# Kernel optimization log

Hardware: AMD Instinct MI355X
Metric: run time of the kernel (lower is better)

## Reference

```python
import jax, jax.numpy as jnp
import numpy as np

N_GRAPHS = 128


def fake_quant4(W):
    # per-tensor symmetric 4-bit weight fake-quant (brevitas-style)
    s = jnp.max(jnp.abs(W)) / 7.0
    q = jnp.clip(jnp.round(W / s), -8.0, 7.0) * s
    # STE: identity gradient through rounding
    return W + jax.lax.stop_gradient(q - W)


def gin_layer(h, src, dst, wa, ba, wb, bb, n_nodes):
    # GIN aggregation: (1+eps)*x + sum_neighbors, eps=0
    agg = jax.ops.segment_sum(h[src], dst, num_segments=n_nodes)  # [N, D]
    h = h + agg
    # int4 weight-only quantized 2-layer MLP
    h = jax.nn.relu(h @ fake_quant4(wa).T + ba)
    return h @ fake_quant4(wb).T + bb


def setup_inputs() -> dict:
    key = jax.random.key(0)
    ks = jax.random.split(key, 16)
    N, E, D = 50000, 800000, 128
    inp = {
        "x": jax.random.normal(ks[0], (N, D), jnp.float32),
        "edge_index": jax.random.randint(ks[1], (2, E), 0, N),
        "batch": jnp.sort(jax.random.randint(ks[2], (N,), 0, N_GRAPHS)),
    }
    for l in range(3):
        inp[f"w{l}a"] = jax.random.normal(ks[3 + 4 * l], (D, D), jnp.float32) * 0.05
        inp[f"b{l}a"] = jnp.zeros((D,), jnp.float32)
        inp[f"w{l}b"] = jax.random.normal(ks[4 + 4 * l], (D, D), jnp.float32) * 0.05
        inp[f"b{l}b"] = jnp.zeros((D,), jnp.float32)
    return inp


def reference(x, edge_index, batch,
              w0a, b0a, w0b, b0b,
              w1a, b1a, w1b, b1b,
              w2a, b2a, w2b, b2b):
    n_nodes = x.shape[0]
    src, dst = edge_index[0], edge_index[1]
    params = [(w0a, b0a, w0b, b0b), (w1a, b1a, w1b, b1b), (w2a, b2a, w2b, b2b)]
    h = x
    for i, (wa, ba, wb, bb) in enumerate(params):
        h = gin_layer(h, src, dst, wa, ba, wb, bb, n_nodes)
        if i < len(params) - 1:
            h = jax.nn.relu(h)  # dropout with p=0 is a no-op
    # global mean pooling over graphs (JK='last')
    sums = jax.ops.segment_sum(h, batch, num_segments=N_GRAPHS)  # [G, D]
    counts = jax.ops.segment_sum(jnp.ones((n_nodes,), h.dtype), batch, num_segments=N_GRAPHS)
    return sums / jnp.maximum(counts, 1.0)[:, None]
```

## Files before the change

kernel.cpp:

```cpp
#include <hip/hip_runtime.h>
#include <math.h>

#define D 128
#define NG 128
#define SLOTS 64

typedef __attribute__((ext_vector_type(8))) unsigned short u16x8;
typedef __attribute__((ext_vector_type(8))) short bf16x8;
typedef __attribute__((ext_vector_type(4))) float f32x4;

__device__ __forceinline__ float bf2f(unsigned short u) {
  return __uint_as_float(((unsigned int)u) << 16);
}
__device__ __forceinline__ unsigned short f2bf(float f) {
  unsigned int u = __float_as_uint(f);
  u += 0x7FFFu + ((u >> 16) & 1u);
  return (unsigned short)(u >> 16);
}

__global__ __launch_bounds__(256) void prep_kernel(
    const float* __restrict__ x, unsigned short* __restrict__ o, int n8,
    const float* __restrict__ w0, const float* __restrict__ w1,
    const float* __restrict__ w2, const float* __restrict__ w3,
    const float* __restrict__ w4, const float* __restrict__ w5,
    unsigned short* __restrict__ qout, int* __restrict__ cnt, int N) {
  int i = blockIdx.x * 256 + threadIdx.x;
  if (i < N) cnt[i] = 0;
  if (i < n8) {
    const float4* xp = reinterpret_cast<const float4*>(x) + (size_t)i * 2;
    float4 a = xp[0], b = xp[1];
    u16x8 v;
    v[0] = f2bf(a.x); v[1] = f2bf(a.y); v[2] = f2bf(a.z); v[3] = f2bf(a.w);
    v[4] = f2bf(b.x); v[5] = f2bf(b.y); v[6] = f2bf(b.z); v[7] = f2bf(b.w);
    *(reinterpret_cast<u16x8*>(o) + i) = v;
  }
  if (blockIdx.x < 6) {
    const float* w;
    switch (blockIdx.x) {
      case 0: w = w0; break;
      case 1: w = w1; break;
      case 2: w = w2; break;
      case 3: w = w3; break;
      case 4: w = w4; break;
      default: w = w5; break;
    }
    unsigned short* q = qout + (size_t)blockIdx.x * (D * D);
    __shared__ float red[256];
    float m = 0.f;
    for (int k = threadIdx.x; k < D * D; k += 256) m = fmaxf(m, fabsf(w[k]));
    red[threadIdx.x] = m;
    __syncthreads();
    for (int s = 128; s > 0; s >>= 1) {
      if (threadIdx.x < s) red[threadIdx.x] = fmaxf(red[threadIdx.x], red[threadIdx.x + s]);
      __syncthreads();
    }
    float s = red[0] / 7.0f;
    for (int k = threadIdx.x; k < D * D; k += 256) {
      float r = rintf(w[k] / s);
      r = fminf(fmaxf(r, -8.f), 7.f);
      q[k] = f2bf((s > 0.f) ? r * s : 0.f);
    }
  }
}

__global__ __launch_bounds__(256) void build_kernel(const int* __restrict__ dst,
                                                    const int* __restrict__ src,
                                                    int* __restrict__ cnt, int* __restrict__ esrc,
                                                    int E, int per_team) {
  int team = blockIdx.x & 7;
  int tb = blockIdx.x >> 3;
  int nb = gridDim.x >> 3;
  int lo = team * per_team;
  int hi = lo + per_team;
  for (int e = tb * 256 + threadIdx.x; e < E; e += nb * 256) {
    int d = dst[e];
    if (d >= lo && d < hi) {
      int slot = atomicAdd(&cnt[d], 1);
      if (slot < SLOTS) esrc[(size_t)d * SLOTS + slot] = src[e];
    }
  }
}

__global__ __launch_bounds__(256) void aggregate_kernel(
    const unsigned short* __restrict__ h, const int* __restrict__ cnt,
    const int* __restrict__ esrc, unsigned short* __restrict__ out, int n) {
  int node = blockIdx.x * 16 + threadIdx.y;
  if (node >= n) return;
  int x = threadIdx.x;
  const u16x8* hp = reinterpret_cast<const u16x8*>(h);
  u16x8 v = hp[(size_t)node * 16 + x];
  float acc[8];
#pragma unroll
  for (int i = 0; i < 8; i++) acc[i] = bf2f(v[i]);
  int c = cnt[node];
  if (c > SLOTS) c = SLOTS;
  const int* base = esrc + (size_t)node * SLOTS;
  int e = 0;
  for (; e + 8 <= c; e += 8) {
    int4 i0 = *reinterpret_cast<const int4*>(base + e);
    int4 i1 = *reinterpret_cast<const int4*>(base + e + 4);
    u16x8 a0 = hp[(size_t)i0.x * 16 + x];
    u16x8 a1 = hp[(size_t)i0.y * 16 + x];
    u16x8 a2 = hp[(size_t)i0.z * 16 + x];
    u16x8 a3 = hp[(size_t)i0.w * 16 + x];
    u16x8 a4 = hp[(size_t)i1.x * 16 + x];
    u16x8 a5 = hp[(size_t)i1.y * 16 + x];
    u16x8 a6 = hp[(size_t)i1.z * 16 + x];
    u16x8 a7 = hp[(size_t)i1.w * 16 + x];
#pragma unroll
    for (int i = 0; i < 8; i++)
      acc[i] += (bf2f(a0[i]) + bf2f(a1[i])) + (bf2f(a2[i]) + bf2f(a3[i])) +
                (bf2f(a4[i]) + bf2f(a5[i])) + (bf2f(a6[i]) + bf2f(a7[i]));
  }
  for (; e + 4 <= c; e += 4) {
    int4 i0 = *reinterpret_cast<const int4*>(base + e);
    u16x8 a0 = hp[(size_t)i0.x * 16 + x];
    u16x8 a1 = hp[(size_t)i0.y * 16 + x];
    u16x8 a2 = hp[(size_t)i0.z * 16 + x];
    u16x8 a3 = hp[(size_t)i0.w * 16 + x];
#pragma unroll
    for (int i = 0; i < 8; i++)
      acc[i] += (bf2f(a0[i]) + bf2f(a1[i])) + (bf2f(a2[i]) + bf2f(a3[i]));
  }
  for (; e < c; e++) {
    u16x8 a0 = hp[(size_t)base[e] * 16 + x];
#pragma unroll
    for (int i = 0; i < 8; i++) acc[i] += bf2f(a0[i]);
  }
  u16x8 r;
#pragma unroll
  for (int i = 0; i < 8; i++) r[i] = f2bf(acc[i]);
  reinterpret_cast<u16x8*>(out)[(size_t)node * 16 + x] = r;
}

__global__ __launch_bounds__(256, 3) void mlp_kernel(
    unsigned short* __restrict__ hio, const unsigned short* __restrict__ W1,
    const float* __restrict__ b1, const unsigned short* __restrict__ W2,
    const float* __restrict__ b2, int N, int relu_out) {
  __shared__ unsigned short Wt[128 * D];
  __shared__ unsigned short hs[4][16 * D];
  const int tid = threadIdx.x;
  const int lane = tid & 63;
  const int w = tid >> 6;
  const int c = lane & 15;
  const int q = lane >> 4;

  const int node = blockIdx.x * 64 + w * 16 + c;

  bf16x8 afrag[4];
  if (node < N) {
    const bf16x8* hp = reinterpret_cast<const bf16x8*>(hio);
    size_t rb = (size_t)node * 16;
#pragma unroll
    for (int ks = 0; ks < 4; ks++) afrag[ks] = hp[rb + ks * 4 + q];
  } else {
#pragma unroll
    for (int ks = 0; ks < 4; ks++)
#pragma unroll
      for (int i = 0; i < 8; i++) afrag[ks][i] = 0;
  }

#pragma unroll
  for (int i = 0; i < 8; i++) {
    int gid = tid + 256 * i;
    int row = gid >> 4;
    int g = gid & 15;
    *reinterpret_cast<u16x8*>(&Wt[row * D + (g ^ (row & 15)) * 8]) =
        *reinterpret_cast<const u16x8*>(W1 + (size_t)row * D + g * 8);
  }
  __syncthreads();

  f32x4 acc1[8] = {};
#pragma unroll
  for (int ks = 0; ks < 4; ks++) {
    int g = ks * 4 + q;
#pragma unroll
    for (int j = 0; j < 8; j++) {
      bf16x8 b = *reinterpret_cast<const bf16x8*>(&Wt[(j * 16 + c) * D + ((g ^ c) * 8)]);
      acc1[j] = __builtin_amdgcn_mfma_f32_16x16x32_bf16(afrag[ks], b, acc1[j], 0, 0, 0);
    }
  }

  unsigned short* tile = &hs[w][0];
#pragma unroll
  for (int j = 0; j < 8; j++) {
    int col = j * 16 + c;
    float bb = b1[col];
    int gcol = col >> 3;
    int el = col & 7;
#pragma unroll
    for (int r = 0; r < 4; r++) {
      int row = q * 4 + r;
      float v = fmaxf(acc1[j][r] + bb, 0.f);
      tile[row * D + ((gcol ^ row) * 8) + el] = f2bf(v);
    }
  }
  __syncthreads();

#pragma unroll
  for (int i = 0; i < 8; i++) {
    int gid = tid + 256 * i;
    int row = gid >> 4;
    int g = gid & 15;
    *reinterpret_cast<u16x8*>(&Wt[row * D + (g ^ (row & 15)) * 8]) =
        *reinterpret_cast<const u16x8*>(W2 + (size_t)row * D + g * 8);
  }
  __syncthreads();

  f32x4 acc2[8] = {};
#pragma unroll
  for (int ks = 0; ks < 4; ks++) {
    int g = ks * 4 + q;
    bf16x8 a = *reinterpret_cast<const bf16x8*>(&tile[c * D + ((g ^ c) * 8)]);
#pragma unroll
    for (int j = 0; j < 8; j++) {
      bf16x8 b = *reinterpret_cast<const bf16x8*>(&Wt[(j * 16 + c) * D + ((g ^ c) * 8)]);
      acc2[j] = __builtin_amdgcn_mfma_f32_16x16x32_bf16(a, b, acc2[j], 0, 0, 0);
    }
  }

#pragma unroll
  for (int j = 0; j < 8; j++) {
    int col = j * 16 + c;
    float bb = b2[col];
#pragma unroll
    for (int r = 0; r < 4; r++) {
      int rnode = blockIdx.x * 64 + w * 16 + q * 4 + r;
      if (rnode < N) {
        float v = acc2[j][r] + bb;
        if (relu_out) v = fmaxf(v, 0.f);
        hio[(size_t)rnode * D + col] = f2bf(v);
      }
    }
  }
}

__global__ __launch_bounds__(256) void pool_partial(const unsigned short* __restrict__ h,
                                                    const int* __restrict__ batch, int n,
                                                    float* __restrict__ partials,
                                                    float* __restrict__ counts) {
  int g = blockIdx.x;
  int s = blockIdx.y;
  __shared__ int sbeg, send;
  if (threadIdx.x == 0) {
    int lo = 0, hi = n;
    while (lo < hi) { int mid = (lo + hi) >> 1; if (batch[mid] < g) lo = mid + 1; else hi = mid; }
    sbeg = lo;
    hi = n;
    while (lo < hi) { int mid = (lo + hi) >> 1; if (batch[mid] < g + 1) lo = mid + 1; else hi = mid; }
    send = lo;
    if (s == 0) counts[g] = (float)(send - sbeg);
  }
  __syncthreads();
  int beg = sbeg, end = send;
  int x = threadIdx.x & 15;
  int ty = threadIdx.x >> 4;
  const u16x8* hp = reinterpret_cast<const u16x8*>(h);
  float acc[8] = {};
  for (int i = beg + s * 16 + ty; i < end; i += 128) {
    u16x8 v = hp[(size_t)i * 16 + x];
#pragma unroll
    for (int k = 0; k < 8; k++) acc[k] += bf2f(v[k]);
  }
  __shared__ float red[16][16][8];
#pragma unroll
  for (int k = 0; k < 8; k++) red[ty][x][k] = acc[k];
  __syncthreads();
  for (int st = 8; st > 0; st >>= 1) {
    if (ty < st) {
#pragma unroll
      for (int k = 0; k < 8; k++) red[ty][x][k] += red[ty + st][x][k];
    }
    __syncthreads();
  }
  if (ty == 0) {
#pragma unroll
    for (int k = 0; k < 8; k++)
      partials[((size_t)s * NG + g) * D + x * 8 + k] = red[0][x][k];
  }
}

__global__ __launch_bounds__(256) void pool_final(const float* __restrict__ partials,
                                                  const float* __restrict__ counts,
                                                  float* __restrict__ out) {
  int idx = blockIdx.x * 256 + threadIdx.x;
  if (idx >= NG * D) return;
  int g = idx >> 7;
  int d = idx & 127;
  float sum = 0.f;
#pragma unroll
  for (int s = 0; s < 8; s++) sum += partials[((size_t)s * NG + g) * D + d];
  out[idx] = sum / fmaxf(counts[g], 1.0f);
}

extern "C" void kernel_launch(void* const* d_in, const int* in_sizes, int n_in,
                              void* d_out, int out_size, void* d_ws, size_t ws_size,
                              hipStream_t stream) {
  const float* x = (const float*)d_in[0];
  const int* ei = (const int*)d_in[1];
  const int* batch = (const int*)d_in[2];
  const float* w[6] = {(const float*)d_in[3], (const float*)d_in[5],
                       (const float*)d_in[7], (const float*)d_in[9],
                       (const float*)d_in[11], (const float*)d_in[13]};
  const float* b[6] = {(const float*)d_in[4], (const float*)d_in[6],
                       (const float*)d_in[8], (const float*)d_in[10],
                       (const float*)d_in[12], (const float*)d_in[14]};
  const int N = in_sizes[0] / D;
  const int E = in_sizes[1] / 2;
  const int* src = ei;
  const int* dst = ei + E;

  char* ws = (char*)d_ws;
  size_t off = 0;
  auto carve = [&](size_t bytes) -> char* {
    char* p = ws + off;
    off = (off + bytes + 255) & ~(size_t)255;
    return p;
  };
  unsigned short* hA = (unsigned short*)carve((size_t)N * D * 2);
  unsigned short* hB = (unsigned short*)carve((size_t)N * D * 2);
  unsigned short* qw = (unsigned short*)carve(6 * D * D * 2);
  int* cnt = (int*)carve((size_t)N * 4);
  int* esrc = (int*)carve((size_t)N * SLOTS * 4);
  float* partials = (float*)carve((size_t)8 * NG * D * 4);
  float* counts = (float*)carve((size_t)NG * 4);
  if (off > ws_size) return;

  int n8 = N * D / 8;
  int prepGrid = (n8 + 255) / 256;
  if (prepGrid < 6) prepGrid = 6;
  int nzGrid = (N + 255) / 256;
  if (prepGrid < nzGrid) prepGrid = nzGrid;
  prep_kernel<<<prepGrid, 256, 0, stream>>>(x, hA, n8, w[0], w[1], w[2], w[3], w[4], w[5], qw, cnt, N);

  int bGrid = ((E + 255) / 256 + 7) & ~7;
  int per_team = (N + 7) / 8;
  build_kernel<<<bGrid, 256, 0, stream>>>(dst, src, cnt, esrc, E, per_team);

  dim3 aggBlock(16, 16);
  int aggGrid = (N + 15) / 16;
  int mlpGrid = (N + 63) / 64;
  unsigned short* cur = hA;
  unsigned short* oth = hB;
  for (int l = 0; l < 3; ++l) {
    aggregate_kernel<<<aggGrid, aggBlock, 0, stream>>>(cur, cnt, esrc, oth, N);
    mlp_kernel<<<mlpGrid, 256, 0, stream>>>(oth, qw + (size_t)(2 * l) * D * D, b[2 * l],
                                            qw + (size_t)(2 * l + 1) * D * D, b[2 * l + 1], N,
                                            (l < 2) ? 1 : 0);
    unsigned short* t = cur; cur = oth; oth = t;
  }

  dim3 ppGrid(NG, 8);
  pool_partial<<<ppGrid, 256, 0, stream>>>(cur, batch, N, partials, counts);
  pool_final<<<(NG * D + 255) / 256, 256, 0, stream>>>(partials, counts, (float*)d_out);
}
```

Baseline: 227.2 us.

## Swizzle block indices across XCDs, prefetch W2, coalesce MLP output stores, widen pooling split

Remaps block indices so consecutive logical blocks land on the same XCD (chiplet), which is meant to improve L2 locality for the prep, aggregate, MLP and pooling kernels. In the MLP kernel, W2 is loaded into registers before the first GEMM so its global latency overlaps compute, and output rows are staged through the swizzled LDS tile so each lane writes 16-byte vectors instead of scattered 2-byte stores. Pooling now splits each graph across 16 slices instead of 8 for more parallelism. The cost is extra register pressure from the W2 prefetch and an LDS round trip on the output path.

Measured after the change: 206.7 us. -9.0%, faster.

```diff
diff --git a/kernel.cpp b/kernel.cpp
--- a/kernel.cpp
+++ b/kernel.cpp
@@ -4,6 +4,7 @@
 #define D 128
 #define NG 128
 #define SLOTS 64
+#define PSPLIT 16
 
 typedef __attribute__((ext_vector_type(8))) unsigned short u16x8;
 typedef __attribute__((ext_vector_type(8))) short bf16x8;
@@ -16,6 +17,13 @@
   unsigned int u = __float_as_uint(f);
   u += 0x7FFFu + ((u >> 16) & 1u);
   return (unsigned short)(u >> 16);
+}
+
+__device__ __forceinline__ int swz_block(int b, int nb) {
+  int xcd = b & 7, idx = b >> 3;
+  int q = nb >> 3, r = nb & 7;
+  int start = xcd * q + (xcd < r ? xcd : r);
+  return start + idx;
 }
 
 __global__ __launch_bounds__(256) void prep_kernel(
@@ -24,7 +32,8 @@
     const float* __restrict__ w2, const float* __restrict__ w3,
     const float* __restrict__ w4, const float* __restrict__ w5,
     unsigned short* __restrict__ qout, int* __restrict__ cnt, int N) {
-  int i = blockIdx.x * 256 + threadIdx.x;
+  int lb = swz_block(blockIdx.x, gridDim.x);
+  int i = lb * 256 + threadIdx.x;
   if (i < N) cnt[i] = 0;
   if (i < n8) {
     const float4* xp = reinterpret_cast<const float4*>(x) + (size_t)i * 2;
@@ -84,7 +93,8 @@
 __global__ __launch_bounds__(256) void aggregate_kernel(
     const unsigned short* __restrict__ h, const int* __restrict__ cnt,
     const int* __restrict__ esrc, unsigned short* __restrict__ out, int n) {
-  int node = blockIdx.x * 16 + threadIdx.y;
+  int lb = swz_block(blockIdx.x, gridDim.x);
+  int node = lb * 16 + threadIdx.y;
   if (node >= n) return;
   int x = threadIdx.x;
   const u16x8* hp = reinterpret_cast<const u16x8*>(h);
@@ -144,8 +154,9 @@
   const int w = tid >> 6;
   const int c = lane & 15;
   const int q = lane >> 4;
-
-  const int node = blockIdx.x * 64 + w * 16 + c;
+  const int lb = swz_block(blockIdx.x, gridDim.x);
+
+  const int node = lb * 64 + w * 16 + c;
 
   bf16x8 afrag[4];
   if (node < N) {
@@ -168,6 +179,14 @@
     *reinterpret_cast<u16x8*>(&Wt[row * D + (g ^ (row & 15)) * 8]) =
         *reinterpret_cast<const u16x8*>(W1 + (size_t)row * D + g * 8);
   }
+  u16x8 w2pre[8];
+#pragma unroll
+  for (int i = 0; i < 8; i++) {
+    int gid = tid + 256 * i;
+    int row = gid >> 4;
+    int g = gid & 15;
+    w2pre[i] = *reinterpret_cast<const u16x8*>(W2 + (size_t)row * D + g * 8);
+  }
   __syncthreads();
 
   f32x4 acc1[8] = {};
@@ -202,8 +221,7 @@
     int gid = tid + 256 * i;
     int row = gid >> 4;
     int g = gid & 15;
-    *reinterpret_cast<u16x8*>(&Wt[row * D + (g ^ (row & 15)) * 8]) =
-        *reinterpret_cast<const u16x8*>(W2 + (size_t)row * D + g * 8);
+    *reinterpret_cast<u16x8*>(&Wt[row * D + (g ^ (row & 15)) * 8]) = w2pre[i];
   }
   __syncthreads();
 
@@ -223,14 +241,27 @@
   for (int j = 0; j < 8; j++) {
     int col = j * 16 + c;
     float bb = b2[col];
+    int gcol = col >> 3;
+    int el = col & 7;
 #pragma unroll
     for (int r = 0; r < 4; r++) {
-      int rnode = blockIdx.x * 64 + w * 16 + q * 4 + r;
-      if (rnode < N) {
-        float v = acc2[j][r] + bb;
-        if (relu_out) v = fmaxf(v, 0.f);
-        hio[(size_t)rnode * D + col] = f2bf(v);
-      }
+      int row = q * 4 + r;
+      float v = acc2[j][r] + bb;
+      if (relu_out) v = fmaxf(v, 0.f);
+      tile[row * D + ((gcol ^ row) * 8) + el] = f2bf(v);
+    }
+  }
+  asm volatile("s_waitcnt lgkmcnt(0)" ::: "memory");
+  __builtin_amdgcn_sched_barrier(0);
+  {
+    int x = lane & 15;
+#pragma unroll
+    for (int i = 0; i < 4; i++) {
+      int row = (lane >> 4) + 4 * i;
+      u16x8 v = *reinterpret_cast<const u16x8*>(&tile[row * D + ((x ^ row) * 8)]);
+      int rnode = lb * 64 + w * 16 + row;
+      if (rnode < N)
+        *reinterpret_cast<u16x8*>(&hio[(size_t)rnode * D + x * 8]) = v;
     }
   }
 }
@@ -239,7 +270,7 @@
                                                     const int* __restrict__ batch, int n,
                                                     float* __restrict__ partials,
                                                     float* __restrict__ counts) {
-  int g = blockIdx.x;
+  int g = swz_block(blockIdx.x, NG);
   int s = blockIdx.y;
   __shared__ int sbeg, send;
   if (threadIdx.x == 0) {
@@ -257,7 +288,7 @@
   int ty = threadIdx.x >> 4;
   const u16x8* hp = reinterpret_cast<const u16x8*>(h);
   float acc[8] = {};
-  for (int i = beg + s * 16 + ty; i < end; i += 128) {
+  for (int i = beg + s * 16 + ty; i < end; i += 16 * PSPLIT) {
     u16x8 v = hp[(size_t)i * 16 + x];
 #pragma unroll
     for (int k = 0; k < 8; k++) acc[k] += bf2f(v[k]);
@@ -289,7 +320,7 @@
   int d = idx & 127;
   float sum = 0.f;
 #pragma unroll
-  for (int s = 0; s < 8; s++) sum += partials[((size_t)s * NG + g) * D + d];
+  for (int s = 0; s < PSPLIT; s++) sum += partials[((size_t)s * NG + g) * D + d];
   out[idx] = sum / fmaxf(counts[g], 1.0f);
 }
 
@@ -322,7 +353,7 @@
   unsigned short* qw = (unsigned short*)carve(6 * D * D * 2);
   int* cnt = (int*)carve((size_t)N * 4);
   int* esrc = (int*)carve((size_t)N * SLOTS * 4);
-  float* partials = (float*)carve((size_t)8 * NG * D * 4);
+  float* partials = (float*)carve((size_t)PSPLIT * NG * D * 4);
   float* counts = (float*)carve((size_t)NG * 4);
   if (off > ws_size) return;
 
@@ -350,7 +381,7 @@
     unsigned short* t = cur; cur = oth; oth = t;
   }
 
-  dim3 ppGrid(NG, 8);
+  dim3 ppGrid(NG, PSPLIT);
   pool_partial<<<ppGrid, 256, 0, stream>>>(cur, batch, N, partials, counts);
   pool_final<<<(NG * D + 255) / 256, 256, 0, stream>>>(partials, counts, (float*)d_out);
 }
```
